# Performance work log

Hardware: AMD Instinct MI355X
Metric: run time of the kernel (lower is better)

## Reference

```python
import jax, jax.numpy as jnp
import numpy as np

LABEL_SIZE = 50
START_IDX, END_IDX, PAD_IDX = 47, 48, 49
B, T, L = 256, 1024, LABEL_SIZE
NEG = -10000.0


def setup_inputs() -> dict:
    key = jax.random.key(0)
    k1, k2, k3, k4 = jax.random.split(key, 4)
    lstm_scores = jax.random.normal(k1, (B, T, L), dtype=jnp.float32)
    transition = jax.random.normal(k2, (L, L), dtype=jnp.float32)
    # replicate the constructor's masking of impossible transitions
    transition = transition.at[:, START_IDX].set(NEG)
    transition = transition.at[END_IDX, :].set(NEG)
    transition = transition.at[:, PAD_IDX].set(NEG)
    transition = transition.at[PAD_IDX, :].set(NEG)
    word_seq_lens = jnp.maximum(jax.random.randint(k3, (B,), 0, T + 1), 1).astype(jnp.int32)
    tags = jax.random.randint(k4, (B, T), 0, START_IDX).astype(jnp.int32)
    mask = (jnp.arange(T)[None, :] < word_seq_lens[:, None])  # (B, T) bool
    return {"lstm_scores": lstm_scores, "transition": transition,
            "word_seq_lens": word_seq_lens, "tags": tags, "mask": mask}


def _crf_nll(lstm_scores, transition, word_seq_lens, tags, mask):
    b, t, l = lstm_scores.shape
    # ---- forward (unlabeled / partition) algorithm via scan over time ----
    alpha0 = transition[START_IDX][None, :] + lstm_scores[:, 0, :]  # (B, L)

    def step(alpha_prev, emit_t):  # emit_t: (B, L)
        # scores[b, i, j] = alpha_prev[b, i] + transition[i, j] + emit_t[b, j]
        s = alpha_prev[:, :, None] + transition[None, :, :] + emit_t[:, None, :]
        alpha = jax.nn.logsumexp(s, axis=1)  # (B, L)
        return alpha, alpha

    emits = jnp.swapaxes(lstm_scores, 0, 1)  # (T, B, L)
    _, alphas_rest = jax.lax.scan(step, alpha0, emits[1:])
    alpha = jnp.concatenate([alpha0[None], alphas_rest], axis=0)  # (T, B, L)

    batch_idx = jnp.arange(b)
    last_alpha = alpha[word_seq_lens - 1, batch_idx]  # (B, L)
    last_alpha = last_alpha + transition[:, END_IDX][None, :]
    unlabeled = jnp.sum(jax.nn.logsumexp(last_alpha, axis=1))

    # ---- labeled (gold path) score ----
    emit_tag = jnp.take_along_axis(lstm_scores, tags[..., None].astype(jnp.int32), axis=2)[..., 0]  # (B, T)
    begin = transition[START_IDX, tags[:, 0]] + emit_tag[:, 0]  # (B,)
    trans_mid = transition[tags[:, :-1], tags[:, 1:]]  # (B, T-1)
    middle = (trans_mid + emit_tag[:, 1:]) * mask[:, 1:].astype(lstm_scores.dtype)
    end_tag = tags[batch_idx, word_seq_lens - 1]  # (B,)
    end = transition[end_tag, END_IDX]
    labeled = jnp.sum(begin) + jnp.sum(end) + jnp.sum(middle)
    return unlabeled, labeled


def reference(lstm_scores, transition, word_seq_lens, tags, mask):
    return _crf_nll(lstm_scores, transition, word_seq_lens, tags, mask)
```

## Files before the change

### kernel.cpp

```cpp
#include <hip/hip_runtime.h>

#define LL 50
#define TT 1024
#define BB 256
#define START_I 47
#define END_I 48
#define NS 48
#define CT 48
#define NCH 21
#define MSTRIDE 2304

typedef __attribute__((ext_vector_type(8))) short bh8;
typedef __attribute__((ext_vector_type(16))) float fx16;
typedef __attribute__((ext_vector_type(4))) unsigned int ux4;

__device__ __forceinline__ unsigned int cvtpk_bf16(float lo, float hi) {
  unsigned int r;
  asm("v_cvt_pk_bf16_f32 %0, %1, %2" : "=v"(r) : "v"(lo), "v"(hi));
  return r;
}
__device__ __forceinline__ void pls(unsigned int& a, unsigned int& b) {
  asm("v_permlane32_swap_b32 %0, %1" : "+v"(a), "+v"(b));
}
__device__ __forceinline__ float rdlane(float v, int i) {
  return __int_as_float(__builtin_amdgcn_readlane(__float_as_int(v), i));
}
#define MFMA __builtin_amdgcn_mfma_f32_32x32x16_bf16

__global__ __launch_bounds__(64) __attribute__((amdgpu_waves_per_eu(4)))
void crf_pass1(const float* __restrict__ lstm, const float* __restrict__ trans,
               float* __restrict__ Mb, int* __restrict__ Mc) {
  const int bk = blockIdx.x;
  const int b = bk / NCH;
  const int k = bk - b * NCH;
  const int lane = threadIdx.x;
  const int h = lane >> 5;
  const int c31 = lane & 31;

  bh8 afr[2][3];
#pragma unroll
  for (int T = 0; T < 2; ++T)
#pragma unroll
    for (int c = 0; c < 3; ++c) {
      float ev[8];
#pragma unroll
      for (int d = 0; d < 8; ++d) {
        int si = 16 * c + 8 * h + d, so = 32 * T + c31;
        ev[d] = (so < LL) ? __expf(trans[si * LL + so]) : 0.f;
      }
      ux4 dw = {cvtpk_bf16(ev[0], ev[1]), cvtpk_bf16(ev[2], ev[3]),
                cvtpk_bf16(ev[4], ev[5]), cvtpk_bf16(ev[6], ev[7])};
      afr[T][c] = __builtin_bit_cast(bh8, dw);
    }

  int ro[24];
#pragma unroll
  for (int r = 0; r < 16; ++r) ro[r] = (r & 3) + 8 * (r >> 2) + 4 * h;
#pragma unroll
  for (int r = 0; r < 8; ++r) ro[16 + r] = 32 + (r & 3) + 8 * (r >> 2) + 4 * h;

  bh8 bq0[3], bq1[3];
#pragma unroll
  for (int kc = 0; kc < 3; ++kc) {
    ux4 w0v, w1v;
#pragma unroll
    for (int wd = 0; wd < 4; ++wd) {
      int lo = 16 * kc + 8 * h + 2 * wd, hi2 = lo + 1;
      int col0 = c31, col1 = 32 + c31;
      w0v[wd] = (lo == col0 ? 0x3F80u : 0u) | (hi2 == col0 ? 0x3F800000u : 0u);
      w1v[wd] = (lo == col1 ? 0x3F80u : 0u) | (hi2 == col1 ? 0x3F800000u : 0u);
    }
    bq0[kc] = __builtin_bit_cast(bh8, w0v);
    bq1[kc] = __builtin_bit_cast(bh8, w1v);
  }

  const float* __restrict__ fb = lstm + ((size_t)b * TT + (1 + k * CT)) * LL;
  float fvA[24], fvB[24];
#pragma unroll
  for (int i = 0; i < 24; ++i) fvA[i] = fb[ro[i]];

  int cnt = 0;
  float d00[16], d01[16], d10[8], d11[8];
  fx16 z16 = {};

  auto STEP = [&](const float (&fv)[24], float (&fn)[24], const float* nrow,
                  bool check) {
    fx16 a00, a01, a10, a11;
    a00 = MFMA(afr[0][0], bq0[0], z16, 0, 0, 0);
    a10 = MFMA(afr[1][0], bq0[0], z16, 0, 0, 0);
    a01 = MFMA(afr[0][0], bq1[0], z16, 0, 0, 0);
    a11 = MFMA(afr[1][0], bq1[0], z16, 0, 0, 0);
    a00 = MFMA(afr[0][1], bq0[1], a00, 0, 0, 0);
    a10 = MFMA(afr[1][1], bq0[1], a10, 0, 0, 0);
    a01 = MFMA(afr[0][1], bq1[1], a01, 0, 0, 0);
    a11 = MFMA(afr[1][1], bq1[1], a11, 0, 0, 0);
    a00 = MFMA(afr[0][2], bq0[2], a00, 0, 0, 0);
    a10 = MFMA(afr[1][2], bq0[2], a10, 0, 0, 0);
    a01 = MFMA(afr[0][2], bq1[2], a01, 0, 0, 0);
    a11 = MFMA(afr[1][2], bq1[2], a11, 0, 0, 0);
#pragma unroll
    for (int i = 0; i < 24; ++i) fn[i] = nrow[ro[i]];
#pragma unroll
    for (int r = 0; r < 16; ++r) {
      float ff = __expf(fv[r]);
      d00[r] = a00[r] * ff;
      d01[r] = a01[r] * ff;
    }
#pragma unroll
    for (int r = 0; r < 8; ++r) {
      float ff = __expf(fv[16 + r]);
      d10[r] = a10[r] * ff;
      d11[r] = a11[r] * ff;
    }
    if (check) {
      float mx = d00[0];
#pragma unroll
      for (int r = 1; r < 16; ++r) mx = fmaxf(mx, d00[r]);
#pragma unroll
      for (int r = 0; r < 16; ++r) mx = fmaxf(mx, d01[r]);
#pragma unroll
      for (int r = 0; r < 8; ++r) mx = fmaxf(mx, fmaxf(d10[r], d11[r]));
      unsigned long long up = __ballot(mx >= 0x1p32f);
      unsigned long long dn = __ballot(mx >= 0x1p-16f);
      if (up) {
#pragma unroll
        for (int r = 0; r < 16; ++r) {
          d00[r] *= 0x1p-64f;
          d01[r] *= 0x1p-64f;
        }
#pragma unroll
        for (int r = 0; r < 8; ++r) {
          d10[r] *= 0x1p-64f;
          d11[r] *= 0x1p-64f;
        }
        cnt += 2;
      } else if (!dn) {
#pragma unroll
        for (int r = 0; r < 16; ++r) {
          d00[r] *= 0x1p32f;
          d01[r] *= 0x1p32f;
        }
#pragma unroll
        for (int r = 0; r < 8; ++r) {
          d10[r] *= 0x1p32f;
          d11[r] *= 0x1p32f;
        }
        cnt -= 1;
      }
    }
    auto PACK = [&](float (&p0)[16], float (&p1)[8], bh8 (&bqo)[3]) {
      unsigned P0[8], P1[4];
#pragma unroll
      for (int p_ = 0; p_ < 8; ++p_) P0[p_] = cvtpk_bf16(p0[2 * p_], p0[2 * p_ + 1]);
#pragma unroll
      for (int p_ = 0; p_ < 4; ++p_) P1[p_] = cvtpk_bf16(p1[2 * p_], p1[2 * p_ + 1]);
      pls(P0[0], P0[2]);
      pls(P0[1], P0[3]);
      pls(P0[4], P0[6]);
      pls(P0[5], P0[7]);
      pls(P1[0], P1[2]);
      pls(P1[1], P1[3]);
      ux4 w0 = {P0[0], P0[1], P0[2], P0[3]};
      ux4 w1 = {P0[4], P0[5], P0[6], P0[7]};
      ux4 w2 = {P1[0], P1[1], P1[2], P1[3]};
      bqo[0] = __builtin_bit_cast(bh8, w0);
      bqo[1] = __builtin_bit_cast(bh8, w1);
      bqo[2] = __builtin_bit_cast(bh8, w2);
    };
    PACK(d00, d10, bq0);
    PACK(d01, d11, bq1);
  };

  for (int uu = 0; uu < CT; uu += 2) {
    STEP(fvA, fvB, fb + (size_t)(uu + 1) * LL, false);
    STEP(fvB, fvA, fb + (size_t)(uu + 2) * LL, true);
  }

  __shared__ float lt[NS][NS + 1];
#pragma unroll
  for (int r = 0; r < 16; ++r) lt[ro[r]][c31] = d00[r];
#pragma unroll
  for (int r = 0; r < 8; ++r) lt[ro[16 + r]][c31] = d10[r];
  if (c31 < 16) {
#pragma unroll
    for (int r = 0; r < 16; ++r) lt[ro[r]][32 + c31] = d01[r];
#pragma unroll
    for (int r = 0; r < 8; ++r) lt[ro[16 + r]][32 + c31] = d11[r];
  }
  __syncthreads();
  float* __restrict__ mg = Mb + ((size_t)b * NCH + k) * MSTRIDE;
  if (lane < NS) {
#pragma unroll
    for (int s = 0; s < NS; ++s) mg[s * NS + lane] = lt[lane][s];
  }
  if (lane == 0) Mc[b * NCH + k] = cnt;
}

__global__ __launch_bounds__(64) __attribute__((amdgpu_waves_per_eu(1, 1)))
void crf_pass2(const float* __restrict__ lstm, const float* __restrict__ trans,
               const int* __restrict__ lens, const int* __restrict__ tags,
               const float* __restrict__ Mb, const int* __restrict__ Mc,
               float* __restrict__ wsf) {
  const int b = blockIdx.x;
  const int lane = threadIdx.x;
  const bool act = lane < NS;
  const int cl = act ? lane : (NS - 1);
  const int len = lens[b];
  const int L = len - 1;
  const int K = L / CT;
  const int r = L - K * CT;

  float e[NS];
#pragma unroll
  for (int i = 0; i < NS; ++i) {
    float ev = __expf(trans[i * LL + cl]);
    e[i] = act ? ev : 0.0f;
  }

  const float* __restrict__ base = lstm + (size_t)b * TT * LL;
  float alpha = act ? __expf(trans[START_I * LL + lane] + base[cl]) : 0.0f;
  int cnt32 = 0;

  const float* __restrict__ mgb = Mb + (size_t)b * NCH * MSTRIDE;
  float mcur[NS], mnxt[NS];
  if (K > 0) {
#pragma unroll
    for (int i = 0; i < NS; ++i) mcur[i] = mgb[i * NS + cl];
  }
  for (int k = 0; k < K; ++k) {
    if (k + 1 < K) {
      const float* mgp = mgb + (size_t)(k + 1) * MSTRIDE;
#pragma unroll
      for (int i = 0; i < NS; ++i) mnxt[i] = mgp[i * NS + cl];
    }
    float a0 = 0.f, a1 = 0.f, a2 = 0.f, a3 = 0.f;
#pragma unroll
    for (int i = 0; i < NS; i += 4) {
      a0 = fmaf(rdlane(alpha, i + 0), mcur[i + 0], a0);
      a1 = fmaf(rdlane(alpha, i + 1), mcur[i + 1], a1);
      a2 = fmaf(rdlane(alpha, i + 2), mcur[i + 2], a2);
      a3 = fmaf(rdlane(alpha, i + 3), mcur[i + 3], a3);
    }
    float an = (a0 + a1) + (a2 + a3);
    unsigned long long up = __ballot(an >= 0x1p64f);
    unsigned long long dn = __ballot(an >= 0x1p-64f);
    float s = up ? 0x1p-64f : (dn ? 1.0f : 0x1p64f);
    cnt32 += up ? 2 : (dn ? 0 : -2);
    alpha = an * s;
    cnt32 += Mc[b * NCH + k];
    if (k + 1 < K) {
#pragma unroll
      for (int i = 0; i < NS; ++i) mcur[i] = mnxt[i];
    }
  }

  auto VSTEP = [&](float em) {
    float f = __expf(em);
    float a0 = 0.f, a1 = 0.f, a2 = 0.f, a3 = 0.f;
#pragma unroll
    for (int i = 0; i < NS; i += 4) {
      a0 = fmaf(rdlane(alpha, i + 0), e[i + 0], a0);
      a1 = fmaf(rdlane(alpha, i + 1), e[i + 1], a1);
      a2 = fmaf(rdlane(alpha, i + 2), e[i + 2], a2);
      a3 = fmaf(rdlane(alpha, i + 3), e[i + 3], a3);
    }
    float qn = ((a0 + a1) + (a2 + a3)) * f;
    unsigned long long up = __ballot(qn >= 0x1p64f);
    unsigned long long dn = __ballot(qn >= 0x1p-64f);
    float s = up ? 0x1p-64f : (dn ? 1.0f : 0x1p64f);
    cnt32 += up ? 2 : (dn ? 0 : -2);
    alpha = qn * s;
  };

  {
    const float* p = base + (size_t)(CT * K + 1) * LL + cl;
    float ebuf[8];
#pragma unroll
    for (int kk = 0; kk < 8; ++kk) ebuf[kk] = p[(size_t)kk * LL];
    int u = 0;
    for (; u + 8 <= r; u += 8) {
#pragma unroll
      for (int s8 = 0; s8 < 8; ++s8) {
        VSTEP(ebuf[s8]);
        int tn = u + s8 + 8;
        tn = (tn < r) ? tn : 0;
        ebuf[s8] = p[(size_t)tn * LL];
      }
    }
    if (u + 0 < r) VSTEP(ebuf[0]);
    if (u + 1 < r) VSTEP(ebuf[1]);
    if (u + 2 < r) VSTEP(ebuf[2]);
    if (u + 3 < r) VSTEP(ebuf[3]);
    if (u + 4 < r) VSTEP(ebuf[4]);
    if (u + 5 < r) VSTEP(ebuf[5]);
    if (u + 6 < r) VSTEP(ebuf[6]);
  }

  float w = 0.0f;
  if (act) w = alpha * __expf(trans[lane * LL + END_I]);
#pragma unroll
  for (int off = 32; off > 0; off >>= 1) w += __shfl_xor(w, off, 64);
  float unl = (float)cnt32 * 22.180709777918249f + __logf(w);

  const int* tg = tags + (size_t)b * TT;
  float lab = 0.0f;
  for (int t0 = 0; t0 < len; t0 += 64) {
    int t = t0 + lane;
    if (t >= 1 && t < len) {
      int tp = tg[t - 1];
      int tc = tg[t];
      lab += trans[tp * LL + tc] + lstm[((size_t)b * TT + t) * LL + tc];
    }
  }
#pragma unroll
  for (int off = 32; off > 0; off >>= 1) lab += __shfl_xor(lab, off, 64);

  if (lane == 0) {
    int tg0 = tg[0];
    float begin = trans[START_I * LL + tg0] + lstm[(size_t)b * TT * LL + tg0];
    int tgl = tg[len - 1];
    float endv = trans[tgl * LL + END_I];
    wsf[b] = unl;
    wsf[BB + b] = lab + begin + endv;
  }
}

__global__ __launch_bounds__(64) __attribute__((amdgpu_waves_per_eu(1, 1)))
void crf_fwd_legacy(
    const float* __restrict__ lstm, const float* __restrict__ trans,
    const int* __restrict__ lens, const int* __restrict__ tags,
    float* __restrict__ ws) {
  const int b = blockIdx.x;
  const int lane = threadIdx.x;
  const bool act = lane < LL;
  const int cl = act ? lane : (LL - 1);
  const int len = lens[b];

  float e[LL];
#pragma unroll
  for (int i = 0; i < LL; ++i) {
    float ev = __expf(trans[i * LL + cl]);
    e[i] = act ? ev : 0.0f;
  }
  const float* __restrict__ base = lstm + (size_t)b * TT * LL + cl;
  float q = act ? __expf(trans[START_I * LL + lane] + base[0]) : 0.0f;
  int cnt = 0;
  float s_pend = 1.0f;

  auto STEP = [&](float em) {
    float f = __expf(em) * s_pend;
    float acc0 = 0.f, acc1 = 0.f, acc2 = 0.f, acc3 = 0.f;
#pragma unroll
    for (int i = 0; i < 48; i += 4) {
      acc0 = fmaf(rdlane(q, i + 0), e[i + 0], acc0);
      acc1 = fmaf(rdlane(q, i + 1), e[i + 1], acc1);
      acc2 = fmaf(rdlane(q, i + 2), e[i + 2], acc2);
      acc3 = fmaf(rdlane(q, i + 3), e[i + 3], acc3);
    }
    acc0 = fmaf(rdlane(q, 48), e[48], acc0);
    acc1 = fmaf(rdlane(q, 49), e[49], acc1);
    float qn = ((acc0 + acc1) + (acc2 + acc3)) * f;
    unsigned long long up = __ballot(qn >= 0x1p64f);
    unsigned long long dn = __ballot(qn >= 0x1p-64f);
    s_pend = up ? 0x1p-64f : (dn ? 1.0f : 0x1p64f);
    cnt += up ? 1 : (dn ? 0 : -1);
    q = qn;
  };

  float ebuf[8];
  const float* p = base + LL;
#pragma unroll
  for (int k = 0; k < 8; ++k) ebuf[k] = p[k * LL];
  const int nb = (len - 1) >> 3;
  const int rem = (len - 1) & 7;
  for (int blk = 0; blk < nb; ++blk) {
    const float* pf = p + 8 * LL;
    if (blk < 126) {
#pragma unroll
      for (int u = 0; u < 8; ++u) {
        STEP(ebuf[u]);
        ebuf[u] = pf[u * LL];
      }
    } else {
#pragma unroll
      for (int u = 0; u < 8; ++u) {
        STEP(ebuf[u]);
        int tn = 9 + 8 * blk + u;
        if (tn < TT) ebuf[u] = pf[u * LL];
      }
    }
    p = pf;
  }
  for (int u = 0; u < rem; ++u) STEP(ebuf[u]);
  q *= s_pend;

  float wv = 0.0f;
  if (act) wv = q * __expf(trans[lane * LL + END_I]);
#pragma unroll
  for (int off = 32; off > 0; off >>= 1) wv += __shfl_xor(wv, off, 64);
  float unl = (float)cnt * 44.361419555836498f + __logf(wv);

  const int* tg = tags + (size_t)b * TT;
  float lab = 0.0f;
  for (int t0 = 0; t0 < len; t0 += 64) {
    int t = t0 + lane;
    if (t >= 1 && t < len) {
      int tp = tg[t - 1];
      int tc = tg[t];
      lab += trans[tp * LL + tc] + lstm[((size_t)b * TT + t) * LL + tc];
    }
  }
#pragma unroll
  for (int off = 32; off > 0; off >>= 1) lab += __shfl_xor(lab, off, 64);

  if (lane == 0) {
    int tg0 = tg[0];
    float begin = trans[START_I * LL + tg0] + lstm[(size_t)b * TT * LL + tg0];
    int tgl = tg[len - 1];
    float endv = trans[tgl * LL + END_I];
    ws[b] = unl;
    ws[BB + b] = lab + begin + endv;
  }
}

__global__ __launch_bounds__(256) void crf_reduce(const float* __restrict__ ws,
                                                  float* __restrict__ out) {
  __shared__ float sm[8];
  int tid = threadIdx.x;
  float u = ws[tid];
  float l = ws[BB + tid];
#pragma unroll
  for (int off = 32; off > 0; off >>= 1) {
    u += __shfl_xor(u, off, 64);
    l += __shfl_xor(l, off, 64);
  }
  int wid = tid >> 6;
  if ((tid & 63) == 0) {
    sm[wid] = u;
    sm[4 + wid] = l;
  }
  __syncthreads();
  if (tid == 0) {
    out[0] = (sm[0] + sm[1]) + (sm[2] + sm[3]);
    out[1] = (sm[4] + sm[5]) + (sm[6] + sm[7]);
  }
}

extern "C" void kernel_launch(void* const* d_in, const int* in_sizes, int n_in,
                              void* d_out, int out_size, void* d_ws, size_t ws_size,
                              hipStream_t stream) {
  const float* lstm = (const float*)d_in[0];
  const float* trans = (const float*)d_in[1];
  const int* lens = (const int*)d_in[2];
  const int* tags = (const int*)d_in[3];
  float* out = (float*)d_out;

  size_t need = (size_t)BB * NCH * MSTRIDE * 4 + (size_t)BB * NCH * 4 +
                (size_t)BB * 2 * 4;
  if (ws_size >= need) {
    float* Mb = (float*)d_ws;
    int* Mc = (int*)(Mb + (size_t)BB * NCH * MSTRIDE);
    float* wsf = (float*)(Mc + BB * NCH);
    crf_pass1<<<dim3(BB * NCH), dim3(64), 0, stream>>>(lstm, trans, Mb, Mc);
    crf_pass2<<<dim3(BB), dim3(64), 0, stream>>>(lstm, trans, lens, tags, Mb, Mc,
                                                 wsf);
    crf_reduce<<<dim3(1), dim3(256), 0, stream>>>(wsf, out);
  } else {
    float* wsf = (float*)d_ws;
    crf_fwd_legacy<<<dim3(BB), dim3(64), 0, stream>>>(lstm, trans, lens, tags, wsf);
    crf_reduce<<<dim3(1), dim3(256), 0, stream>>>(wsf, out);
  }
}
```

Before: 181.3 us.

## Precompute bf16 exp of emissions in a prep kernel and lengthen pass1 chunks

Adds a separate kernel that computes exp of each emission score once and stores it as packed bf16 pairs. Pass1 then loads these with vectorized uint2 reads instead of gathering floats and running expf on every step of the serial MFMA chain. Chunk length also grows from 48 to 64 steps, so there are fewer chunks for pass2 to combine. In exchange there is an extra kernel launch plus a write and re-read of a large workspace buffer, and emission factors lose precision by going through bf16.

```diff
diff --git a/kernel.cpp b/kernel.cpp
--- a/kernel.cpp
+++ b/kernel.cpp
@@ -6,8 +6,8 @@
 #define START_I 47
 #define END_I 48
 #define NS 48
-#define CT 48
-#define NCH 21
+#define CT 64
+#define NCH 15
 #define MSTRIDE 2304
 
 typedef __attribute__((ext_vector_type(8))) short bh8;
@@ -25,10 +25,21 @@
 __device__ __forceinline__ float rdlane(float v, int i) {
   return __int_as_float(__builtin_amdgcn_readlane(__float_as_int(v), i));
 }
+__device__ __forceinline__ float blo(unsigned u) { return __uint_as_float(u << 16); }
+__device__ __forceinline__ float bhi(unsigned u) { return __uint_as_float(u & 0xFFFF0000u); }
 #define MFMA __builtin_amdgcn_mfma_f32_32x32x16_bf16
 
+__global__ __launch_bounds__(256) void crf_prep_exp(
+    const float* __restrict__ lstm, unsigned* __restrict__ fexp) {
+  int flat = blockIdx.x * 256 + threadIdx.x;
+  int bt = flat / 24;
+  int s2 = flat - bt * 24;
+  const float* row = lstm + (size_t)bt * LL + 2 * s2;
+  fexp[flat] = cvtpk_bf16(__expf(row[0]), __expf(row[1]));
+}
+
 __global__ __launch_bounds__(64) __attribute__((amdgpu_waves_per_eu(4)))
-void crf_pass1(const float* __restrict__ lstm, const float* __restrict__ trans,
+void crf_pass1(const unsigned* __restrict__ fexp, const float* __restrict__ trans,
                float* __restrict__ Mb, int* __restrict__ Mc) {
   const int bk = blockIdx.x;
   const int b = bk / NCH;
@@ -74,17 +85,23 @@
     bq1[kc] = __builtin_bit_cast(bh8, w1v);
   }
 
-  const float* __restrict__ fb = lstm + ((size_t)b * TT + (1 + k * CT)) * LL;
-  float fvA[24], fvB[24];
-#pragma unroll
-  for (int i = 0; i < 24; ++i) fvA[i] = fb[ro[i]];
+  const uint2* __restrict__ fp = (const uint2*)fexp;
+  int qoff[6];
+#pragma unroll
+  for (int q = 0; q < 4; ++q) qoff[q] = 2 * q + h;
+#pragma unroll
+  for (int q = 4; q < 6; ++q) qoff[q] = 8 + 2 * (q - 4) + h;
+
+  const size_t bt0 = (size_t)b * TT + 1 + k * CT;
+  uint2 fuA[6], fuB[6];
+#pragma unroll
+  for (int q = 0; q < 6; ++q) fuA[q] = fp[bt0 * 12 + qoff[q]];
 
   int cnt = 0;
   float d00[16], d01[16], d10[8], d11[8];
   fx16 z16 = {};
 
-  auto STEP = [&](const float (&fv)[24], float (&fn)[24], const float* nrow,
-                  bool check) {
+  auto STEP = [&](const uint2 (&fu)[6], uint2 (&fn)[6], size_t btn, bool check) {
     fx16 a00, a01, a10, a11;
     a00 = MFMA(afr[0][0], bq0[0], z16, 0, 0, 0);
     a10 = MFMA(afr[1][0], bq0[0], z16, 0, 0, 0);
@@ -99,18 +116,24 @@
     a01 = MFMA(afr[0][2], bq1[2], a01, 0, 0, 0);
     a11 = MFMA(afr[1][2], bq1[2], a11, 0, 0, 0);
 #pragma unroll
-    for (int i = 0; i < 24; ++i) fn[i] = nrow[ro[i]];
+    for (int q = 0; q < 6; ++q) fn[q] = fp[btn * 12 + qoff[q]];
+    float ff[24];
+#pragma unroll
+    for (int q = 0; q < 6; ++q) {
+      ff[4 * q + 0] = blo(fu[q].x);
+      ff[4 * q + 1] = bhi(fu[q].x);
+      ff[4 * q + 2] = blo(fu[q].y);
+      ff[4 * q + 3] = bhi(fu[q].y);
+    }
 #pragma unroll
     for (int r = 0; r < 16; ++r) {
-      float ff = __expf(fv[r]);
-      d00[r] = a00[r] * ff;
-      d01[r] = a01[r] * ff;
+      d00[r] = a00[r] * ff[r];
+      d01[r] = a01[r] * ff[r];
     }
 #pragma unroll
     for (int r = 0; r < 8; ++r) {
-      float ff = __expf(fv[16 + r]);
-      d10[r] = a10[r] * ff;
-      d11[r] = a11[r] * ff;
+      d10[r] = a10[r] * ff[16 + r];
+      d11[r] = a11[r] * ff[16 + r];
     }
     if (check) {
       float mx = d00[0];
@@ -172,8 +195,8 @@
   };
 
   for (int uu = 0; uu < CT; uu += 2) {
-    STEP(fvA, fvB, fb + (size_t)(uu + 1) * LL, false);
-    STEP(fvB, fvA, fb + (size_t)(uu + 2) * LL, true);
+    STEP(fuA, fuB, bt0 + uu + 1, false);
+    STEP(fuB, fuA, bt0 + uu + 2, true);
   }
 
   __shared__ float lt[NS][NS + 1];
@@ -455,13 +478,16 @@
   const int* tags = (const int*)d_in[3];
   float* out = (float*)d_out;
 
-  size_t need = (size_t)BB * NCH * MSTRIDE * 4 + (size_t)BB * NCH * 4 +
-                (size_t)BB * 2 * 4;
+  const size_t fexpN = (size_t)BB * TT * 24;
+  const size_t MbN = (size_t)BB * NCH * MSTRIDE;
+  size_t need = fexpN * 4 + MbN * 4 + (size_t)BB * NCH * 4 + (size_t)BB * 2 * 4;
   if (ws_size >= need) {
-    float* Mb = (float*)d_ws;
-    int* Mc = (int*)(Mb + (size_t)BB * NCH * MSTRIDE);
+    unsigned* fexp = (unsigned*)d_ws;
+    float* Mb = (float*)(fexp + fexpN);
+    int* Mc = (int*)(Mb + MbN);
     float* wsf = (float*)(Mc + BB * NCH);
-    crf_pass1<<<dim3(BB * NCH), dim3(64), 0, stream>>>(lstm, trans, Mb, Mc);
+    crf_prep_exp<<<dim3(BB * TT * 24 / 256), dim3(256), 0, stream>>>(lstm, fexp);
+    crf_pass1<<<dim3(BB * NCH), dim3(64), 0, stream>>>(fexp, trans, Mb, Mc);
     crf_pass2<<<dim3(BB), dim3(64), 0, stream>>>(lstm, trans, lens, tags, Mb, Mc,
                                                  wsf);
     crf_reduce<<<dim3(1), dim3(256), 0, stream>>>(wsf, out);
```

New measurement: 154.8 us. 1.17x faster.
